# Kernel tuning notes

Hardware: AMD Instinct MI355X
Metric: run time of the kernel (lower is better)

The kernel has to match this reference:

```python
import jax, jax.numpy as jnp
import numpy as np

EPS = 1e-8
EPS12 = 1e-12
TAU = 0.2
IOU_THRESHOLD = 0.5
NEG_INF = -1e9

N, C = 8192, 1024
HID, FGD, CLSD = 256, 64, 128


def setup_inputs() -> dict:
    key = jax.random.key(0)
    ks = jax.random.split(key, 16)
    roi_feats = jax.random.normal(ks[0], (N, C), dtype=jnp.float32)
    # labels in {-1 (ignore), 0 (bg), 1..20 (classes)}
    labels = jax.random.randint(ks[1], (N,), 0, 21, dtype=jnp.int64) - 1
    ious = jax.random.uniform(ks[2], (N,), dtype=jnp.float32)
    s = 0.02
    w1f = jax.random.normal(ks[3], (HID, C), dtype=jnp.float32) * s
    b1f = jnp.zeros((HID,), dtype=jnp.float32)
    w2f = jax.random.normal(ks[4], (FGD, HID), dtype=jnp.float32) * s
    b2f = jnp.zeros((FGD,), dtype=jnp.float32)
    w1c = jax.random.normal(ks[5], (HID, C), dtype=jnp.float32) * s
    b1c = jnp.zeros((HID,), dtype=jnp.float32)
    w2c = jax.random.normal(ks[6], (CLSD, HID), dtype=jnp.float32) * s
    b2c = jnp.zeros((CLSD,), dtype=jnp.float32)
    return {"roi_feats": roi_feats, "labels": labels, "ious": ious,
            "w1f": w1f, "b1f": b1f, "w2f": w2f, "b2f": b2f,
            "w1c": w1c, "b1c": b1c, "w2c": w2c, "b2c": b2c}


def _project_normalize(x, w1, b1, w2, b2):
    h = jax.nn.relu(x @ w1.T + b1)
    z = h @ w2.T + b2
    nrm = jnp.linalg.norm(z, axis=1, keepdims=True)  # F.normalize: z / max(||z||, eps)
    return z / jnp.maximum(nrm, EPS)


def _fg_bg_loss(z_fg, fg_mask, ignore_mask, iou_weight):
    n = z_fg.shape[0]
    anchor = fg_mask & ~ignore_mask
    eye = jnp.eye(n, dtype=bool)
    # pos_mask[i,j] = fg_mask[j] & ~ignore[j], self excluded
    pos = (fg_mask & ~ignore_mask)[None, :] & ~eye  # [N,N]
    sim = (z_fg @ z_fg.T) / TAU
    sim_exp = jnp.exp(sim) * (~eye).astype(sim.dtype)
    denom = sim_exp.sum(axis=1)  # [N]
    numer = jnp.sum(jnp.exp(sim) * pos.astype(sim.dtype), axis=1)  # [N]
    n_pos = pos.sum(axis=1)
    loss_i = -jnp.log((numer + EPS) / (denom + EPS))
    valid = anchor & (n_pos > 0)
    w = iou_weight
    num = jnp.sum(jnp.where(valid, loss_i * w, 0.0))
    den = jnp.sum(jnp.where(valid, w, 0.0)) + EPS
    return num / den


def _class_supcon_loss(z_cls, labels, fg_mask, ignore_mask, iou_weight):
    n = z_cls.shape[0]
    anchor = fg_mask & ~ignore_mask
    eye = jnp.eye(n, dtype=bool)
    valid_den = ~eye & ~ignore_mask[None, :]  # [N,N]
    # pos[i,j]: same label, j not ignored, labels[j] != 0, j != i, j valid
    pos = (labels[None, :] == labels[:, None]) & ~ignore_mask[None, :] & (labels[None, :] != 0)
    pos = pos & ~eye & valid_den
    sim = (z_cls @ z_cls.T) / TAU
    logits = jnp.where(valid_den, sim, NEG_INF)
    denom_log = jax.nn.logsumexp(logits, axis=1)  # [N]
    n_pos = pos.sum(axis=1)
    sum_pos = jnp.sum(jnp.where(pos, sim, 0.0), axis=1)
    n_pos_safe = jnp.maximum(n_pos, 1).astype(sim.dtype)
    loss_i = -(sum_pos - n_pos.astype(sim.dtype) * denom_log) / n_pos_safe
    valid = anchor & (n_pos > 0) & valid_den.any(axis=1)
    w = iou_weight
    num = jnp.sum(jnp.where(valid, loss_i * w, 0.0))
    den = jnp.sum(jnp.where(valid, w, 0.0)) + EPS12
    return num / den


def reference(roi_feats, labels, ious, w1f, b1f, w2f, b2f, w1c, b1c, w2c, b2c):
    z_fg = _project_normalize(roi_feats, w1f, b1f, w2f, b2f)
    z_cls = _project_normalize(roi_feats, w1c, b1c, w2c, b2c)
    ignore_mask = labels == -1
    bg_mask = (labels == 0) & ~ignore_mask
    fg_mask = (labels > 0) & ~ignore_mask
    iou_weight = jnp.where(ious > IOU_THRESHOLD, ious, 0.0)
    loss_fg_bg = _fg_bg_loss(z_fg, fg_mask, ignore_mask, iou_weight)
    loss_supcon = _class_supcon_loss(z_cls, labels, fg_mask, ignore_mask, iou_weight)
    # loss_weights = (1.0, 1.0); stacked as [loss_fg_bg, loss_supcon]
    return jnp.stack([loss_fg_bg * 1.0, loss_supcon * 1.0])
```

## Files before the change

kernel.cpp:

```cpp
#include <hip/hip_runtime.h>
#include <hip/hip_bf16.h>
#include <math.h>

#define N_ROI 8192
#define C_IN  1024
#define HIDD  256
#define FGD   64
#define CLSD  128
#define INV_TAU 5.0f
#define SCALE_LOG2E 7.2134752f
#define LN2F 0.69314718f

using frag_ab = __attribute__((ext_vector_type(8))) short;
using f32x16  = __attribute__((ext_vector_type(16))) float;

static __device__ __forceinline__ short f32_to_bf16_bits(float f) {
  unsigned u = __builtin_bit_cast(unsigned, f);
  u = (u + 0x7FFFu + ((u >> 16) & 1u)) >> 16;
  return (short)u;
}
static __device__ __forceinline__ float bf16_bits_to_f32(short b) {
  unsigned u = ((unsigned)(unsigned short)b) << 16;
  return __builtin_bit_cast(float, u);
}
static __device__ __forceinline__ float fast_exp2(float x) {
#if __has_builtin(__builtin_amdgcn_exp2f)
  return __builtin_amdgcn_exp2f(x);
#else
  return exp2f(x);
#endif
}
static __device__ __forceinline__ void async_copy16(const void* g, void* l) {
  __builtin_amdgcn_global_load_lds(
      (const __attribute__((address_space(1))) unsigned int*)g,
      (__attribute__((address_space(3))) unsigned int*)l, 16, 0, 0);
}

__global__ __launch_bounds__(256) void pack_zero_kernel(
    const float* __restrict__ w1f, const float* __restrict__ w1c,
    const float* __restrict__ w2f, const float* __restrict__ w2c,
    short* __restrict__ W1pf, short* __restrict__ W1pc,
    short* __restrict__ W2pf, short* __restrict__ W2pc,
    float* __restrict__ accum, int* __restrict__ cnt) {
  int b = blockIdx.x;
  if (b == 280) {
    int t = threadIdx.x;
    if (t < 8) accum[t] = 0.f;
    if (t < 24) cnt[t] = 0;
    return;
  }
  const float* src; short* dst; int Ksh; int b0;
  if (b < 128)      { src = w1f; dst = W1pf; Ksh = 10; b0 = 0; }
  else if (b < 256) { src = w1c; dst = W1pc; Ksh = 10; b0 = 128; }
  else if (b < 264) { src = w2f; dst = W2pf; Ksh = 8;  b0 = 256; }
  else              { src = w2c; dst = W2pc; Ksh = 8;  b0 = 264; }
  int K = 1 << Ksh;
  int f = (b - b0) * 256 + threadIdx.x;
  int r = f >> (Ksh - 3);
  int c0 = (f & ((K >> 3) - 1)) << 3;
  float4 v0 = *(const float4*)(src + (size_t)r * K + c0);
  float4 v1 = *(const float4*)(src + (size_t)r * K + c0 + 4);
  union { short s[8]; uint4 v; } o;
  o.s[0] = f32_to_bf16_bits(v0.x); o.s[1] = f32_to_bf16_bits(v0.y);
  o.s[2] = f32_to_bf16_bits(v0.z); o.s[3] = f32_to_bf16_bits(v0.w);
  o.s[4] = f32_to_bf16_bits(v1.x); o.s[5] = f32_to_bf16_bits(v1.y);
  o.s[6] = f32_to_bf16_bits(v1.z); o.s[7] = f32_to_bf16_bits(v1.w);
  ((uint4*)dst)[(size_t)((r >> 5) * (K >> 4) + (c0 >> 4)) * 64 +
                ((c0 >> 3) & 1) * 32 + (r & 31)] = o.v;
}

template<int D>
__device__ __forceinline__ void gemm2_from_lds(
    const short* __restrict__ T2,
    const short* __restrict__ W2p, const float* __restrict__ b2,
    short* __restrict__ Zr, float* __restrict__ tii,
    short* __restrict__ T, int gt) {
  int lane = threadIdx.x & 63;
  const frag_ab* Wv = (const frag_ab*)W2p;
  constexpr int NT = D / 32;
  frag_ab a[16];
  #pragma unroll
  for (int kc = 0; kc < 16; ++kc)
    a[kc] = *(const frag_ab*)&T2[(lane & 31) * 264 + kc * 16 + (lane >> 5) * 8];
  f32x16 acc[NT];
  #pragma unroll
  for (int j = 0; j < NT; ++j)
    #pragma unroll
    for (int q = 0; q < 16; ++q) acc[j][q] = 0.f;
  #pragma unroll
  for (int kc = 0; kc < 16; ++kc)
    #pragma unroll
    for (int j = 0; j < NT; ++j)
      acc[j] = __builtin_amdgcn_mfma_f32_32x32x16_bf16(a[kc], Wv[(j * 16 + kc) * 64 + lane], acc[j], 0, 0, 0);
  int c = lane & 31, h = lane >> 5;
  float bb[NT];
  #pragma unroll
  for (int j = 0; j < NT; ++j) bb[j] = b2[j * 32 + c];
  float s1[16];
  #pragma unroll
  for (int r = 0; r < 16; ++r) {
    s1[r] = 0.f;
    #pragma unroll
    for (int j = 0; j < NT; ++j) {
      float v = acc[j][r] + bb[j];
      s1[r] += v * v;
    }
  }
  #pragma unroll
  for (int r = 0; r < 16; ++r)
    #pragma unroll
    for (int m = 1; m < 32; m <<= 1) s1[r] += __shfl_xor(s1[r], m);
  float s2[16];
  #pragma unroll
  for (int r = 0; r < 16; ++r) s2[r] = 0.f;
  #pragma unroll
  for (int j = 0; j < NT; ++j) {
    int cl = j * 32 + c;
    #pragma unroll
    for (int g = 0; g < 4; ++g) {
      short q0, q1, q2, q3;
      #pragma unroll
      for (int e = 0; e < 4; ++e) {
        int r = g * 4 + e;
        float sc = 1.f / fmaxf(sqrtf(s1[r]), 1e-8f);
        short qb = f32_to_bf16_bits((acc[j][r] + bb[j]) * sc);
        float zf = bf16_bits_to_f32(qb);
        s2[r] += zf * zf;
        if (e == 0) q0 = qb; else if (e == 1) q1 = qb; else if (e == 2) q2 = qb; else q3 = qb;
      }
      *(short4*)&T[cl * 36 + 4 * h + 8 * g] = make_short4(q0, q1, q2, q3);
    }
  }
  #pragma unroll
  for (int r = 0; r < 16; ++r)
    #pragma unroll
    for (int m = 1; m < 32; m <<= 1) s2[r] += __shfl_xor(s2[r], m);
  if (c == 0) {
    #pragma unroll
    for (int r = 0; r < 16; ++r)
      tii[gt * 32 + (r & 3) + 8 * (r >> 2) + 4 * h] = s2[r];
  }
  uint4* Zv = (uint4*)Zr;
  #pragma unroll
  for (int k = 0; k < D / 16; ++k) {
    int c0 = (2 * k + h) * 8;
    union { short s[8]; uint4 u; } o;
    #pragma unroll
    for (int e = 0; e < 8; ++e) o.s[e] = T[(c0 + e) * 36 + c];
    Zv[(size_t)(gt * (D / 16) + k) * 64 + h * 32 + c] = o.u;
  }
}

__global__ __launch_bounds__(256) void fused_mlp_kernel(
    const float* __restrict__ X,
    const short* __restrict__ W1pf, const short* __restrict__ W1pc,
    const float* __restrict__ b1f, const float* __restrict__ b1c,
    const short* __restrict__ W2pf, const short* __restrict__ W2pc,
    const float* __restrict__ b2f, const float* __restrict__ b2c,
    short* __restrict__ Zrf, short* __restrict__ Zrc,
    float* __restrict__ tiif, float* __restrict__ tiic,
    const int* __restrict__ labels,
    float* __restrict__ Sfg, float* __restrict__ Pfg,
    float* __restrict__ Scls, float* __restrict__ SPc,
    float* __restrict__ pfv, float* __restrict__ nimv,
    float* __restrict__ ljmv, int* __restrict__ cnt) {
  __shared__ short stageA[2][1024];
  __shared__ short T2[32 * 264];
  __shared__ short Tw[128 * 36];
  int tid = threadIdx.x, lane = tid & 63, wv = tid >> 6;
  int Mb = blockIdx.x, head = blockIdx.y;

  if (head == 0 && tid < 32) {
    int i = Mb * 32 + tid;
    Sfg[i] = 0.f; Pfg[i] = 0.f; Scls[i] = 0.f; SPc[i] = 0.f;
    int l = labels[i];
    pfv[i]  = (l > 0)  ? 1.f : 0.f;
    nimv[i] = (l != -1) ? 1.f : 0.f;
    ljmv[i] = (l > 0)  ? (float)l : -7.f;
    int b = l + 1; if (b < 0) b = 0; if (b > 21) b = 21;
    atomicAdd(&cnt[b], 1);
  }

  const short* Wp = head ? W1pc : W1pf;
  const float* b1 = head ? b1c  : b1f;
  const uint4* Wv4 = (const uint4*)Wp;
  int arow = tid >> 3;
  int ac4  = tid & 7;
  const float* Xp = X + (size_t)(Mb * 32 + arow) * C_IN + ac4 * 4;
  int aslot = ((ac4 >> 2) * 64 + ((ac4 >> 1) & 1) * 32 + arow) * 8 + (ac4 & 1) * 4;

  float4 av;
  frag_ab breg[2][4];
  f32x16 acc[2];
  #pragma unroll
  for (int nt = 0; nt < 2; ++nt)
    #pragma unroll
    for (int q = 0; q < 16; ++q) acc[nt][q] = 0.f;

  auto loadA = [&](int c) { av = *(const float4*)(Xp + c * 32); };
  auto loadB = [&](int c, int s) {
    #pragma unroll
    for (int kci = 0; kci < 2; ++kci)
      #pragma unroll
      for (int nt = 0; nt < 2; ++nt)
        breg[s][kci * 2 + nt] =
            *(const frag_ab*)&Wv4[(size_t)((wv * 2 + nt) * 64 + c * 2 + kci) * 64 + lane];
  };
  auto storeA = [&](int buf) {
    *(short4*)&stageA[buf][aslot] =
        make_short4(f32_to_bf16_bits(av.x), f32_to_bf16_bits(av.y),
                    f32_to_bf16_bits(av.z), f32_to_bf16_bits(av.w));
  };
  auto domfma = [&](int buf, int bank) {
    frag_ab a0 = *(const frag_ab*)&stageA[buf][(0 * 64 + lane) * 8];
    frag_ab a1 = *(const frag_ab*)&stageA[buf][(1 * 64 + lane) * 8];
    #pragma unroll
    for (int nt = 0; nt < 2; ++nt)
      acc[nt] = __builtin_amdgcn_mfma_f32_32x32x16_bf16(a0, breg[bank][nt], acc[nt], 0, 0, 0);
    #pragma unroll
    for (int nt = 0; nt < 2; ++nt)
      acc[nt] = __builtin_amdgcn_mfma_f32_32x32x16_bf16(a1, breg[bank][2 + nt], acc[nt], 0, 0, 0);
  };

  loadA(0); loadB(0, 0); storeA(0);
  __syncthreads();
  for (int c = 0; c < 32; c += 2) {
    if (c + 1 < 32) { loadA(c + 1); loadB(c + 1, 1); }
    domfma(0, 0);
    if (c + 1 < 32) storeA(1);
    __syncthreads();
    if (c + 2 < 32) { loadA(c + 2); loadB(c + 2, 0); }
    domfma(1, 1);
    if (c + 2 < 32) storeA(0);
    __syncthreads();
  }
  {
    int cl31 = lane & 31, h = lane >> 5;
    #pragma unroll
    for (int nt = 0; nt < 2; ++nt) {
      int gc = wv * 64 + nt * 32 + cl31;
      float bb = b1[gc];
      #pragma unroll
      for (int q = 0; q < 16; ++q) {
        int row = (q & 3) + 8 * (q >> 2) + 4 * h;
        float x = fmaxf(acc[nt][q] + bb, 0.f);
        T2[row * 264 + gc] = f32_to_bf16_bits(x);
      }
    }
  }
  __syncthreads();

  if (wv == 0) {
    if (head == 0)
      gemm2_from_lds<FGD>(T2, W2pf, b2f, Zrf, tiif, Tw, Mb);
    else
      gemm2_from_lds<CLSD>(T2, W2pc, b2c, Zrc, tiic, Tw, Mb);
  }
}

template<int D, int MODE, int NJT>
__device__ __forceinline__ void loss_body(
    const short* __restrict__ Zr, const int* __restrict__ labels,
    const float* __restrict__ pfv, const float* __restrict__ nimv,
    const float* __restrict__ ljmv,
    float* __restrict__ Sg, float* __restrict__ Pg,
    short* __restrict__ smem) {
  constexpr int KC = D / 16;
  constexpr int TSH = KC * 64 * 8;
  constexpr int LD = (KC * 64) / 256;
  int tid = threadIdx.x, lane = tid & 63, wv = tid >> 6;
  int itile = (blockIdx.x >> 1) * 4 + wv;
  int jt0 = blockIdx.y * NJT;
  int jlane = lane & 31;
  const frag_ab* Zrv = (const frag_ab*)Zr;

  frag_ab a[KC];
  #pragma unroll
  for (int kc = 0; kc < KC; ++kc) {
    frag_ab t = Zrv[(itile * KC + kc) * 64 + lane];
    #pragma unroll
    for (int e = 0; e < 8; ++e)
      t[e] = f32_to_bf16_bits(bf16_bits_to_f32(t[e]) * SCALE_LOG2E);
    a[kc] = t;
  }
  float limf[16];
  if (MODE == 1) {
    #pragma unroll
    for (int r = 0; r < 16; ++r) {
      int row = (r & 3) + 8 * (r >> 2) + 4 * (lane >> 5);
      limf[r] = (float)labels[itile * 32 + row];
    }
  }
  asm volatile("s_waitcnt vmcnt(0)" ::: "memory");

  short* b0 = smem;
  short* b1 = smem + TSH;
  short* b2 = smem + 2 * TSH;
  float* maskf = (float*)(smem + 3 * TSH);

  if (MODE == 0) {
    if (tid < 128)
      async_copy16(pfv + jt0 * 32 + tid * 4, maskf + wv * 256);
  } else {
    if (tid < 128)
      async_copy16(nimv + jt0 * 32 + tid * 4, maskf + wv * 256);
    else
      async_copy16(ljmv + jt0 * 32 + (tid - 128) * 4, maskf + 512 + (wv - 2) * 256);
  }

  auto STAGE = [&](short* dst, int kk) {
    const short* src = Zr + (size_t)(jt0 + kk) * KC * 512;
    #pragma unroll
    for (int u = 0; u < LD; ++u)
      async_copy16(src + (size_t)(u * 256 + tid) * 8,
                   dst + (u * 256 + (wv * 64)) * 8);
  };

  STAGE(b0, 0); STAGE(b1, 1);

  float Ssum[16] = {}, Psum[16] = {};

  #pragma unroll 1
  for (int t = 0; t < NJT; ++t) {
    if (t < NJT - 1) {
      if (LD == 1) asm volatile("s_waitcnt vmcnt(1)" ::: "memory");
      else         asm volatile("s_waitcnt vmcnt(2)" ::: "memory");
    } else {
      asm volatile("s_waitcnt vmcnt(0)" ::: "memory");
    }
    __builtin_amdgcn_s_barrier();
    __builtin_amdgcn_sched_barrier(0);
    if (t + 2 < NJT) STAGE(b2, t + 2);

    float pf = 0.f, nim = 0.f, ljm = 0.f;
    if (MODE == 0) pf = maskf[t * 32 + jlane];
    else { nim = maskf[t * 32 + jlane]; ljm = maskf[512 + t * 32 + jlane]; }

    f32x16 acc;
    #pragma unroll
    for (int q = 0; q < 16; ++q) acc[q] = 0.f;
    __builtin_amdgcn_s_setprio(1);
    #pragma unroll
    for (int kc = 0; kc < KC; ++kc) {
      frag_ab b = *(const frag_ab*)&b0[(kc * 64 + lane) * 8];
      acc = __builtin_amdgcn_mfma_f32_32x32x16_bf16(a[kc], b, acc, 0, 0, 0);
    }
    __builtin_amdgcn_s_setprio(0);
    #pragma unroll
    for (int rr = 0; rr < 16; ++rr) {
      float e = fast_exp2(acc[rr]);
      if (MODE == 0) {
        Ssum[rr] += e;
        Psum[rr] = fmaf(pf, e, Psum[rr]);
      } else {
        Ssum[rr] = fmaf(nim, e, Ssum[rr]);
        Psum[rr] += (limf[rr] == ljm) ? acc[rr] : 0.f;
      }
    }
    short* tmp = b0; b0 = b1; b1 = b2; b2 = tmp;
  }

  #pragma unroll
  for (int r = 0; r < 16; ++r) {
    float s = Ssum[r], p = Psum[r];
    #pragma unroll
    for (int m = 1; m < 32; m <<= 1) { s += __shfl_xor(s, m); p += __shfl_xor(p, m); }
    if ((lane & 31) == 0) {
      if (MODE == 1) p *= LN2F;
      int row = (r & 3) + 8 * (r >> 2) + 4 * (lane >> 5);
      atomicAdd(&Sg[itile * 32 + row], s);
      atomicAdd(&Pg[itile * 32 + row], p);
    }
  }
}

__global__ __launch_bounds__(256, 4) void loss_kernel(
    const short* __restrict__ Zrf, const short* __restrict__ Zrc,
    const int* __restrict__ labels,
    const float* __restrict__ pfv, const float* __restrict__ nimv,
    const float* __restrict__ ljmv,
    float* __restrict__ Sfg, float* __restrict__ Pfg,
    float* __restrict__ Scls, float* __restrict__ SPc) {
  __shared__ short smem[3 * 8 * 64 * 8 + 2048];
  if ((blockIdx.x & 1) == 0)
    loss_body<FGD, 0, 16>(Zrf, labels, pfv, nimv, ljmv, Sfg, Pfg, smem);
  else
    loss_body<CLSD, 1, 16>(Zrc, labels, pfv, nimv, ljmv, Scls, SPc, smem);
}

__global__ __launch_bounds__(256) void finalize_kernel(
    const float* __restrict__ Sfg, const float* __restrict__ Pfg,
    const float* __restrict__ Scls, const float* __restrict__ SPc,
    const float* __restrict__ tiif, const float* __restrict__ tiic,
    const int* __restrict__ labels, const float* __restrict__ ious,
    int* __restrict__ cnt, float* __restrict__ accum, float* __restrict__ out) {
  int i = blockIdx.x * 256 + threadIdx.x;
  int l = labels[i];
  float iv = ious[i];
  float w = (iv > 0.5f) ? iv : 0.f;
  int cntP = 0;
  #pragma unroll
  for (int b = 2; b <= 21; ++b) cntP += cnt[b];
  int cntNI = N_ROI - cnt[0];
  bool Pi = (l > 0);
  float numF = 0.f, denF = 0.f, numC = 0.f, denC = 0.f;
  float eF = __expf(INV_TAU * tiif[i]);
  float Sf = Sfg[i] - eF;
  float Pf = Pfg[i] - (Pi ? eF : 0.f);
  int nposF = cntP - (Pi ? 1 : 0);
  if (Pi && nposF > 0) {
    float lossF = logf((Sf + 1e-8f) / (Pf + 1e-8f));
    numF = lossF * w; denF = w;
  }
  float tC = INV_TAU * tiic[i];
  float eC = __expf(tC);
  float Sc = Scls[i] - ((l != -1) ? eC : 0.f);
  float SP = SPc[i] - (Pi ? tC : 0.f);
  int nposC = Pi ? (cnt[l + 1] - 1) : 0;
  bool anyv = (cntNI - ((l != -1) ? 1 : 0)) > 0;
  if (Pi && nposC > 0 && anyv) {
    float lse = logf(Sc);
    float lossC = -(SP - (float)nposC * lse) / fmaxf((float)nposC, 1.f);
    numC = lossC * w; denC = w;
  }
  float v0 = numF, v1 = denF, v2 = numC, v3 = denC;
  #pragma unroll
  for (int m = 1; m < 64; m <<= 1) {
    v0 += __shfl_xor(v0, m); v1 += __shfl_xor(v1, m);
    v2 += __shfl_xor(v2, m); v3 += __shfl_xor(v3, m);
  }
  __shared__ float red[4][4];
  int lane = threadIdx.x & 63, wid = threadIdx.x >> 6;
  if (lane == 0) { red[wid][0]=v0; red[wid][1]=v1; red[wid][2]=v2; red[wid][3]=v3; }
  __syncthreads();
  if (threadIdx.x == 0) {
    float s0=0,s1=0,s2=0,s3=0;
    for (int q = 0; q < 4; ++q) { s0+=red[q][0]; s1+=red[q][1]; s2+=red[q][2]; s3+=red[q][3]; }
    atomicAdd(&accum[0], s0); atomicAdd(&accum[1], s1);
    atomicAdd(&accum[2], s2); atomicAdd(&accum[3], s3);
    __threadfence();
    int t = atomicAdd(&cnt[22], 1);
    if (t == 31) {
      __threadfence();
      out[0] = accum[0] / (accum[1] + 1e-8f);
      out[1] = accum[2] / (accum[3] + 1e-12f);
    }
  }
}

extern "C" void kernel_launch(void* const* d_in, const int* in_sizes, int n_in,
                              void* d_out, int out_size, void* d_ws, size_t ws_size,
                              hipStream_t stream) {
  const float* X    = (const float*)d_in[0];
  const int*  labels= (const int*)d_in[1];
  const float* ious = (const float*)d_in[2];
  const float* w1f  = (const float*)d_in[3];
  const float* b1f  = (const float*)d_in[4];
  const float* w2f  = (const float*)d_in[5];
  const float* b2f  = (const float*)d_in[6];
  const float* w1c  = (const float*)d_in[7];
  const float* b1c  = (const float*)d_in[8];
  const float* w2c  = (const float*)d_in[9];
  const float* b2c  = (const float*)d_in[10];
  float* out = (float*)d_out;

  char* w = (char*)d_ws;
  short* W1pf = (short*)w;            w += 524288;
  short* W1pc = (short*)w;            w += 524288;
  short* W2pf = (short*)w;            w += 32768;
  short* W2pc = (short*)w;            w += 65536;
  short* Zrf  = (short*)w;            w += 1048576;
  short* Zrc  = (short*)w;            w += 2097152;
  float* Sfg  = (float*)w;            w += 32768;
  float* Pfg  = (float*)w;            w += 32768;
  float* Scls = (float*)w;            w += 32768;
  float* SPc  = (float*)w;            w += 32768;
  float* tiif = (float*)w;            w += 32768;
  float* tiic = (float*)w;            w += 32768;
  float* pfv  = (float*)w;            w += 32768;
  float* nimv = (float*)w;            w += 32768;
  float* ljmv = (float*)w;            w += 32768;
  float* accum= (float*)w;            w += 32;
  int*   cnt  = (int*)w;              w += 96;

  pack_zero_kernel<<<281, 256, 0, stream>>>(w1f, w1c, w2f, w2c,
                                            W1pf, W1pc, W2pf, W2pc, accum, cnt);

  fused_mlp_kernel<<<dim3(256, 2), 256, 0, stream>>>(X, W1pf, W1pc, b1f, b1c,
                                            W2pf, W2pc, b2f, b2c,
                                            Zrf, Zrc, tiif, tiic,
                                            labels, Sfg, Pfg, Scls, SPc,
                                            pfv, nimv, ljmv, cnt);

  loss_kernel<<<dim3(128, 16), 256, 0, stream>>>(Zrf, Zrc, labels, pfv, nimv, ljmv,
                                                 Sfg, Pfg, Scls, SPc);

  finalize_kernel<<<N_ROI/256, 256, 0, stream>>>(Sfg, Pfg, Scls, SPc, tiif, tiic,
                                                 labels, ious, cnt, accum, out);
}
```

Before: 187.9 us.

## Use 512-thread loss blocks with two j-tiles per iteration for the fg head

```diff
diff --git a/kernel.cpp b/kernel.cpp
--- a/kernel.cpp
+++ b/kernel.cpp
@@ -266,10 +266,11 @@
     float* __restrict__ Sg, float* __restrict__ Pg,
     short* __restrict__ smem) {
   constexpr int KC = D / 16;
-  constexpr int TSH = KC * 64 * 8;
-  constexpr int LD = (KC * 64) / 256;
+  constexpr int JP = (MODE == 0) ? 2 : 1;
+  constexpr int NIT = NJT / JP;
+  constexpr int BUF_SH = 4096;
   int tid = threadIdx.x, lane = tid & 63, wv = tid >> 6;
-  int itile = (blockIdx.x >> 1) * 4 + wv;
+  int itile = (blockIdx.x >> 1) * 8 + wv;
   int jt0 = blockIdx.y * NJT;
   int jlane = lane & 31;
   const frag_ab* Zrv = (const frag_ab*)Zr;
@@ -291,29 +292,27 @@
       limf[r] = (float)labels[itile * 32 + row];
     }
   }
+  __builtin_amdgcn_sched_barrier(0);
   asm volatile("s_waitcnt vmcnt(0)" ::: "memory");
+  __builtin_amdgcn_sched_barrier(0);
 
   short* b0 = smem;
-  short* b1 = smem + TSH;
-  short* b2 = smem + 2 * TSH;
-  float* maskf = (float*)(smem + 3 * TSH);
+  short* b1 = smem + BUF_SH;
+  short* b2 = smem + 2 * BUF_SH;
+  float* maskf = (float*)(smem + 3 * BUF_SH);
 
   if (MODE == 0) {
-    if (tid < 128)
-      async_copy16(pfv + jt0 * 32 + tid * 4, maskf + wv * 256);
+    async_copy16(pfv + jt0 * 32 + (size_t)(tid & 127) * 4,
+                 maskf + (wv & 1) * 256);
   } else {
-    if (tid < 128)
-      async_copy16(nimv + jt0 * 32 + tid * 4, maskf + wv * 256);
-    else
-      async_copy16(ljmv + jt0 * 32 + (tid - 128) * 4, maskf + 512 + (wv - 2) * 256);
-  }
-
-  auto STAGE = [&](short* dst, int kk) {
-    const short* src = Zr + (size_t)(jt0 + kk) * KC * 512;
-    #pragma unroll
-    for (int u = 0; u < LD; ++u)
-      async_copy16(src + (size_t)(u * 256 + tid) * 8,
-                   dst + (u * 256 + (wv * 64)) * 8);
+    const float* msrc = ((wv & 2) == 0) ? nimv : ljmv;
+    float* mdst = maskf + ((wv & 2) ? 512 : 0) + (wv & 1) * 256;
+    async_copy16(msrc + jt0 * 32 + (size_t)(tid & 127) * 4, mdst);
+  }
+
+  auto STAGE = [&](short* dst, int it) {
+    const short* src = Zr + (size_t)(jt0 + it * JP) * KC * 512 / JP * JP;
+    async_copy16(src + (size_t)tid * 8, dst + wv * 512);
   };
 
   STAGE(b0, 0); STAGE(b1, 1);
@@ -321,38 +320,51 @@
   float Ssum[16] = {}, Psum[16] = {};
 
   #pragma unroll 1
-  for (int t = 0; t < NJT; ++t) {
-    if (t < NJT - 1) {
-      if (LD == 1) asm volatile("s_waitcnt vmcnt(1)" ::: "memory");
-      else         asm volatile("s_waitcnt vmcnt(2)" ::: "memory");
-    } else {
-      asm volatile("s_waitcnt vmcnt(0)" ::: "memory");
-    }
+  for (int t = 0; t < NIT; ++t) {
+    if (t < NIT - 1) asm volatile("s_waitcnt vmcnt(1)" ::: "memory");
+    else             asm volatile("s_waitcnt vmcnt(0)" ::: "memory");
     __builtin_amdgcn_s_barrier();
     __builtin_amdgcn_sched_barrier(0);
-    if (t + 2 < NJT) STAGE(b2, t + 2);
-
-    float pf = 0.f, nim = 0.f, ljm = 0.f;
-    if (MODE == 0) pf = maskf[t * 32 + jlane];
-    else { nim = maskf[t * 32 + jlane]; ljm = maskf[512 + t * 32 + jlane]; }
-
-    f32x16 acc;
-    #pragma unroll
-    for (int q = 0; q < 16; ++q) acc[q] = 0.f;
-    __builtin_amdgcn_s_setprio(1);
-    #pragma unroll
-    for (int kc = 0; kc < KC; ++kc) {
-      frag_ab b = *(const frag_ab*)&b0[(kc * 64 + lane) * 8];
-      acc = __builtin_amdgcn_mfma_f32_32x32x16_bf16(a[kc], b, acc, 0, 0, 0);
-    }
-    __builtin_amdgcn_s_setprio(0);
-    #pragma unroll
-    for (int rr = 0; rr < 16; ++rr) {
-      float e = fast_exp2(acc[rr]);
-      if (MODE == 0) {
-        Ssum[rr] += e;
-        Psum[rr] = fmaf(pf, e, Psum[rr]);
-      } else {
+    if (t + 2 < NIT) STAGE(b2, t + 2);
+
+    if (MODE == 0) {
+      float pf0 = maskf[t * 64 + jlane];
+      float pf1 = maskf[t * 64 + 32 + jlane];
+      f32x16 acc0, acc1;
+      #pragma unroll
+      for (int q = 0; q < 16; ++q) { acc0[q] = 0.f; acc1[q] = 0.f; }
+      __builtin_amdgcn_s_setprio(1);
+      #pragma unroll
+      for (int kc = 0; kc < KC; ++kc) {
+        frag_ab bb0 = *(const frag_ab*)&b0[(kc * 64 + lane) * 8];
+        frag_ab bb1 = *(const frag_ab*)&b0[((KC + kc) * 64 + lane) * 8];
+        acc0 = __builtin_amdgcn_mfma_f32_32x32x16_bf16(a[kc], bb0, acc0, 0, 0, 0);
+        acc1 = __builtin_amdgcn_mfma_f32_32x32x16_bf16(a[kc], bb1, acc1, 0, 0, 0);
+      }
+      __builtin_amdgcn_s_setprio(0);
+      #pragma unroll
+      for (int rr = 0; rr < 16; ++rr) {
+        float e0 = fast_exp2(acc0[rr]);
+        float e1 = fast_exp2(acc1[rr]);
+        Ssum[rr] += e0 + e1;
+        Psum[rr] = fmaf(pf0, e0, fmaf(pf1, e1, Psum[rr]));
+      }
+    } else {
+      float nim = maskf[t * 32 + jlane];
+      float ljm = maskf[512 + t * 32 + jlane];
+      f32x16 acc;
+      #pragma unroll
+      for (int q = 0; q < 16; ++q) acc[q] = 0.f;
+      __builtin_amdgcn_s_setprio(1);
+      #pragma unroll
+      for (int kc = 0; kc < KC; ++kc) {
+        frag_ab b = *(const frag_ab*)&b0[(kc * 64 + lane) * 8];
+        acc = __builtin_amdgcn_mfma_f32_32x32x16_bf16(a[kc], b, acc, 0, 0, 0);
+      }
+      __builtin_amdgcn_s_setprio(0);
+      #pragma unroll
+      for (int rr = 0; rr < 16; ++rr) {
+        float e = fast_exp2(acc[rr]);
         Ssum[rr] = fmaf(nim, e, Ssum[rr]);
         Psum[rr] += (limf[rr] == ljm) ? acc[rr] : 0.f;
       }
@@ -374,14 +386,14 @@
   }
 }
 
-__global__ __launch_bounds__(256, 4) void loss_kernel(
+__global__ __launch_bounds__(512, 2) void loss_kernel(
     const short* __restrict__ Zrf, const short* __restrict__ Zrc,
     const int* __restrict__ labels,
     const float* __restrict__ pfv, const float* __restrict__ nimv,
     const float* __restrict__ ljmv,
     float* __restrict__ Sfg, float* __restrict__ Pfg,
     float* __restrict__ Scls, float* __restrict__ SPc) {
-  __shared__ short smem[3 * 8 * 64 * 8 + 2048];
+  __shared__ short smem[3 * 4096 + 2048];
   if ((blockIdx.x & 1) == 0)
     loss_body<FGD, 0, 16>(Zrf, labels, pfv, nimv, ljmv, Sfg, Pfg, smem);
   else
@@ -492,8 +504,8 @@
                                             labels, Sfg, Pfg, Scls, SPc,
                                             pfv, nimv, ljmv, cnt);
 
-  loss_kernel<<<dim3(128, 16), 256, 0, stream>>>(Zrf, Zrc, labels, pfv, nimv, ljmv,
-                                                 Sfg, Pfg, Scls, SPc);
+  loss_kernel<<<dim3(64, 16), 512, 0, stream>>>(Zrf, Zrc, labels, pfv, nimv, ljmv,
+                                                Sfg, Pfg, Scls, SPc);
 
   finalize_kernel<<<N_ROI/256, 256, 0, stream>>>(Sfg, Pfg, Scls, SPc, tiif, tiic,
                                                  labels, ious, cnt, accum, out);
```

New measurement: 190.2 us. No clear change (+1.2%).
